# Optimization experiments

Measured on AMD Instinct MI355X. Metric: run time of the kernel, lower is better.

Reference implementation:

```python
import jax, jax.numpy as jnp
import numpy as np


def _register_translation(target_images, src_images, upsample_factor):
    # squeeze channel dim -> (B, H, W), promote to complex for FFT
    tgt = target_images[..., 0].astype(jnp.complex64)
    src = src_images[..., 0].astype(jnp.complex64)
    B, H, W = tgt.shape

    target_freq = jnp.fft.fft2(tgt)
    src_freq = jnp.fft.fft2(src)
    # cross-power spectrum (skimage register_translation convention)
    image_product = src_freq * jnp.conj(target_freq)
    cross_corr = jnp.fft.ifft2(image_product)

    # coarse (integer-pixel) peak
    abs_cc = jnp.abs(cross_corr).reshape(B, -1)
    idx = jnp.argmax(abs_cc, axis=1)
    maxima = jnp.stack([idx // W, idx % W], axis=1).astype(jnp.float32)  # (B,2)
    shape_f = jnp.array([H, W], jnp.float32)
    midpoints = jnp.array([H // 2, W // 2], jnp.float32)  # fix(axis_size/2)
    shifts = jnp.where(maxima > midpoints, maxima - shape_f, maxima)

    if upsample_factor > 1:
        uf = float(upsample_factor)
        shifts = jnp.round(shifts * uf) / uf
        region = int(np.ceil(upsample_factor * 1.5))  # upsampled region size
        dftshift = float(np.fix(region / 2.0))
        offsets = dftshift - shifts * uf  # (B,2) sample region offsets

        r_idx = jnp.arange(region, dtype=jnp.float32)
        freq_r = (jnp.fft.fftfreq(H) * H).astype(jnp.float32)  # ifftshift(arange(H)-H//2)
        freq_c = (jnp.fft.fftfreq(W) * W).astype(jnp.float32)
        two_pi = 2.0 * np.pi

        # per-batch small DFT kernels: row (B, region, H), col (B, W, region)
        row_ang = (two_pi / (H * uf)) * (r_idx[None, :, None] - offsets[:, 0][:, None, None]) * freq_r[None, None, :]
        col_ang = (two_pi / (W * uf)) * freq_c[None, :, None] * (r_idx[None, None, :] - offsets[:, 1][:, None, None])
        row_k = jnp.exp(-1j * row_ang)
        col_k = jnp.exp(-1j * col_ang)

        # upsampled DFT of conj(image_product), then conjugate back
        cc_up = jnp.conj(jnp.einsum('brh,bhw,bwc->brc', row_k, jnp.conj(image_product), col_k))
        abs_up = jnp.abs(cc_up).reshape(B, -1)
        idx2 = jnp.argmax(abs_up, axis=1)
        max2 = jnp.stack([idx2 // region, idx2 % region], axis=1).astype(jnp.float32) - dftshift
        shifts = shifts + max2 / uf

    return shifts  # (B, 2) -- (row_shift, col_shift)


def setup_inputs() -> dict:
    key = jax.random.key(0)
    k1, k2 = jax.random.split(key)
    B, H, W = 32, 512, 512
    target_images = jax.random.normal(k1, (B, H, W, 1), dtype=jnp.float32)
    src_images = jax.random.normal(k2, (B, H, W, 1), dtype=jnp.float32)
    return {"target_images": target_images, "src_images": src_images, "upsample_factor": 20}


def reference(target_images, src_images, upsample_factor):
    return _register_translation(target_images, src_images, upsample_factor)
```

## Files before the change

kernel.cpp:

```cpp
#include <hip/hip_runtime.h>
#include <math.h>

#define BN 32
#define HN 512
#define WN 512
#define REGION 30
#define RPAD 32
#define UFV 20.0f
#define DFTSHIFT 15.0f
#define TWO_PI 6.2831853071795864769f
#define HS 8
#define HCH (HN / HS)
#define WS 8
#define WCH (WN / WS)

typedef float2 cplx;

__device__ __forceinline__ cplx cmul(cplx a, cplx b){
    return make_float2(a.x*b.x - a.y*b.y, a.x*b.y + a.y*b.x);
}
__device__ __forceinline__ cplx cadd(cplx a, cplx b){
    return make_float2(a.x + b.x, a.y + b.y);
}
__device__ __forceinline__ cplx csub(cplx a, cplx b){
    return make_float2(a.x - b.x, a.y - b.y);
}
__device__ __forceinline__ int brev9(int i){ return (int)(__brev((unsigned)i) >> 23); }
__device__ __forceinline__ int brev6(int i){ return (int)(__brev((unsigned)i) >> 26); }
__device__ __forceinline__ int csl(int h, int c){ return c * 546 + h + (h >> 4); }

#define BFLY(a,b,w){ cplx t_ = cmul(w,b); b = make_float2(a.x - t_.x, a.y - t_.y); a = cadd(a, t_); }
#define BFLY1(a,b){ cplx t_ = b; b = make_float2(a.x - t_.x, a.y - t_.y); a = cadd(a, t_); }

__device__ __forceinline__ void fft512_regs(cplx* v, const float2* tw, cplx* ds, int lane){
    const cplx wI  = *(const cplx*)&tw[128];
    const cplx w8a = *(const cplx*)&tw[64];
    const cplx w8b = *(const cplx*)&tw[192];
    BFLY1(v[0],v[1]); BFLY1(v[2],v[3]); BFLY1(v[4],v[5]); BFLY1(v[6],v[7]);
    BFLY1(v[0],v[2]); BFLY(v[1],v[3],wI); BFLY1(v[4],v[6]); BFLY(v[5],v[7],wI);
    BFLY1(v[0],v[4]); BFLY(v[1],v[5],w8a); BFLY(v[2],v[6],wI); BFLY(v[3],v[7],w8b);
    const int h = lane >> 3, lo = lane & 7;
    const int bw = 9 * lane;
    const int br = 72 * h + lo;
    #pragma unroll
    for (int j = 0; j < 8; ++j) ds[bw + j] = v[j];
    asm volatile("s_waitcnt lgkmcnt(0)" ::: "memory");
    #pragma unroll
    for (int j = 0; j < 8; ++j) v[j] = ds[br + 9*j];
    {
        cplx wA = *(const cplx*)&tw[lo<<5];
        BFLY(v[0],v[1],wA); BFLY(v[2],v[3],wA); BFLY(v[4],v[5],wA); BFLY(v[6],v[7],wA);
        cplx wB0 = *(const cplx*)&tw[lo<<4], wB1 = *(const cplx*)&tw[128+(lo<<4)];
        BFLY(v[0],v[2],wB0); BFLY(v[1],v[3],wB1); BFLY(v[4],v[6],wB0); BFLY(v[5],v[7],wB1);
        cplx wC0 = *(const cplx*)&tw[lo<<3], wC1 = *(const cplx*)&tw[64+(lo<<3)];
        cplx wC2 = *(const cplx*)&tw[128+(lo<<3)], wC3 = *(const cplx*)&tw[192+(lo<<3)];
        BFLY(v[0],v[4],wC0); BFLY(v[1],v[5],wC1); BFLY(v[2],v[6],wC2); BFLY(v[3],v[7],wC3);
    }
    #pragma unroll
    for (int j = 0; j < 8; ++j) ds[br + 9*j] = v[j];
    asm volatile("s_waitcnt lgkmcnt(0)" ::: "memory");
    const int br3 = lane + (lane >> 3);
    #pragma unroll
    for (int j = 0; j < 8; ++j) v[j] = ds[br3 + 72*j];
    {
        cplx wD = *(const cplx*)&tw[lane<<2];
        BFLY(v[0],v[1],wD); BFLY(v[2],v[3],wD); BFLY(v[4],v[5],wD); BFLY(v[6],v[7],wD);
        cplx wE0 = *(const cplx*)&tw[lane<<1], wE1 = *(const cplx*)&tw[128+(lane<<1)];
        BFLY(v[0],v[2],wE0); BFLY(v[1],v[3],wE1); BFLY(v[4],v[6],wE0); BFLY(v[5],v[7],wE1);
        cplx wF0 = *(const cplx*)&tw[lane], wF1 = *(const cplx*)&tw[64+lane];
        cplx wF2 = *(const cplx*)&tw[128+lane], wF3 = *(const cplx*)&tw[192+lane];
        BFLY(v[0],v[4],wF0); BFLY(v[1],v[5],wF1); BFLY(v[2],v[6],wF2); BFLY(v[3],v[7],wF3);
    }
}

__global__ void __launch_bounds__(256) row_fft_pack(const float* __restrict__ tgt,
                                                    const float* __restrict__ src,
                                                    cplx* __restrict__ Fz){
    __shared__ float2 tw[256];
    __shared__ cplx ds[4 * 576];
    const int tid = threadIdx.x;
    { float sv, cv; sincosf(-TWO_PI * (float)tid * (1.0f/512.0f), &sv, &cv);
      tw[tid] = make_float2(cv, sv); }
    __syncthreads();
    const int wave = tid >> 6, lane = tid & 63;
    const int rid = blockIdx.x * 4 + wave;
    const float* tr = tgt + (size_t)rid * WN;
    const float* sr = src + (size_t)rid * WN;
    const int rb6 = brev6(lane);
    const int B3[8] = {0,256,128,384,64,320,192,448};
    cplx v[8];
    #pragma unroll
    for (int j = 0; j < 8; ++j){ int o = B3[j] + rb6; v[j] = make_float2(tr[o], sr[o]); }
    fft512_regs(v, (const float2*)tw, ds + wave * 576, lane);
    cplx* orow = Fz + (size_t)rid * WN;
    #pragma unroll
    for (int j = 0; j < 8; ++j) orow[64*j + lane] = v[j];
}

__device__ __forceinline__ void col_fft8(cplx* sm, const float2* tw, int tid){
    const cplx wI  = tw[128];
    const cplx w8a = tw[64];
    const cplx w8b = tw[192];
    const int c  = tid & 7;
    const int k0 = tid >> 3, k1 = k0 + 32;
    const int B3[8] = {0,256,128,384,64,320,192,448};
    cplx ya[8], yb[8];
    {
        const int r0 = brev6(k0), r1 = brev6(k1);
        #pragma unroll
        for (int m = 0; m < 8; ++m){
            ya[m] = sm[csl(B3[m] + r0, c)];
            yb[m] = sm[csl(B3[m] + r1, c)];
        }
    }
    __syncthreads();
    #define P0(x) \
        BFLY1(x[0],x[1]); BFLY1(x[2],x[3]); BFLY1(x[4],x[5]); BFLY1(x[6],x[7]); \
        BFLY1(x[0],x[2]); BFLY(x[1],x[3],wI); BFLY1(x[4],x[6]); BFLY(x[5],x[7],wI); \
        BFLY1(x[0],x[4]); BFLY(x[1],x[5],w8a); BFLY(x[2],x[6],wI); BFLY(x[3],x[7],w8b);
    P0(ya); P0(yb);
    #undef P0
    #pragma unroll
    for (int m = 0; m < 8; ++m){
        sm[csl(8*k0 + m, c)] = ya[m];
        sm[csl(8*k1 + m, c)] = yb[m];
    }
    __syncthreads();
    #pragma unroll
    for (int pass = 1; pass < 3; ++pass){
        const int st = 3*pass + 1;
        const int h1 = 1 << (st - 1);
        #pragma unroll
        for (int gi = 0; gi < 2; ++gi){
            const int k = (tid >> 3) + 32*gi;
            const int q = k & (h1 - 1);
            const int i0 = ((k >> (st - 1)) << (st + 2)) + q;
            cplx x[8];
            #pragma unroll
            for (int m = 0; m < 8; ++m) x[m] = sm[csl(i0 + m*h1, c)];
            cplx w1 = tw[q << (9 - st)];
            BFLY(x[0],x[1],w1); BFLY(x[2],x[3],w1); BFLY(x[4],x[5],w1); BFLY(x[6],x[7],w1);
            cplx w2a = tw[q << (8 - st)];
            cplx w2b = tw[(q << (8 - st)) + 128];
            BFLY(x[0],x[2],w2a); BFLY(x[1],x[3],w2b); BFLY(x[4],x[6],w2a); BFLY(x[5],x[7],w2b);
            cplx w30 = tw[q << (7 - st)];
            cplx w31 = tw[(q << (7 - st)) + 64];
            cplx w32 = tw[(q << (7 - st)) + 128];
            cplx w33 = tw[(q << (7 - st)) + 192];
            BFLY(x[0],x[4],w30); BFLY(x[1],x[5],w31); BFLY(x[2],x[6],w32); BFLY(x[3],x[7],w33);
            #pragma unroll
            for (int m = 0; m < 8; ++m) sm[csl(i0 + m*h1, c)] = x[m];
        }
        __syncthreads();
    }
}

__global__ void col_fft_fwd(cplx* __restrict__ buf){
    const int b  = blockIdx.y;
    const int w0 = blockIdx.x * 8;
    const int tid = threadIdx.x;
    __shared__ cplx sm[4368];
    __shared__ float2 tw[256];
    { float sv, cv; sincosf(-TWO_PI * (float)tid * (1.0f/512.0f), &sv, &cv);
      tw[tid] = make_float2(cv, sv); }
    cplx* base = buf + (size_t)b * HN * WN + w0;
    for (int idx = tid; idx < HN * 4; idx += 256){
        int h = idx >> 2, c2 = (idx & 3) << 1;
        float4 v = *(const float4*)(base + (size_t)h * WN + c2);
        sm[csl(h, c2)]     = make_float2(v.x, v.y);
        sm[csl(h, c2 + 1)] = make_float2(v.z, v.w);
    }
    __syncthreads();
    col_fft8(sm, (const float2*)tw, tid);
    for (int idx = tid; idx < HN * 4; idx += 256){
        int h = idx >> 2, c2 = (idx & 3) << 1;
        cplx a = sm[csl(h, c2)], d = sm[csl(h, c2 + 1)];
        *(float4*)(base + (size_t)h * WN + c2) = make_float4(a.x, a.y, d.x, d.y);
    }
}

__global__ void __launch_bounds__(256) cross_rowinv(cplx* __restrict__ Fz, cplx* __restrict__ cc){
    __shared__ float2 tw[256];
    __shared__ cplx ds[4 * 1184];
    const int tid = threadIdx.x;
    { float sv, cv; sincosf(TWO_PI * (float)tid * (1.0f/512.0f), &sv, &cv);
      tw[tid] = make_float2(cv, sv); }
    __syncthreads();
    const int wave = tid >> 6, lane = tid & 63;
    const int p = blockIdx.x * 4 + wave;
    if (p > 256) return;
    const int b = blockIdx.y;
    const int h1 = p, h2 = (HN - p) & (HN - 1);
    cplx* r1 = Fz + ((size_t)b * HN + h1) * WN;
    cplx* r2 = Fz + ((size_t)b * HN + h2) * WN;
    cplx* A = ds + wave * 1184;
    cplx* B = A + 592;
    #pragma unroll
    for (int u = 0; u < 8; ++u){
        A[lane + 64*u] = r1[lane + 64*u];
        B[lane + 64*u] = r2[lane + 64*u];
    }
    asm volatile("s_waitcnt lgkmcnt(0)" ::: "memory");
    const int rb6 = brev6(lane);
    const int B3[8] = {0,256,128,384,64,320,192,448};
    cplx v1[8], v2[8];
    #pragma unroll
    for (int j = 0; j < 8; ++j){
        int w  = B3[j] + rb6;
        int wm = (WN - w) & (WN - 1);
        cplx Aw = A[w], Bw = B[w], Am = A[wm], Bm = B[wm];
        { cplx Bc = make_float2(Bm.x, -Bm.y);
          cplx s = cadd(Aw, Bc);
          cplx d = make_float2(Aw.x - Bc.x, Aw.y - Bc.y);
          cplx D = make_float2(d.x*s.x + d.y*s.y, d.y*s.x - d.x*s.y);
          v1[j] = make_float2(0.25f * D.y, -0.25f * D.x); }
        { cplx Ac = make_float2(Am.x, -Am.y);
          cplx s = cadd(Bw, Ac);
          cplx d = make_float2(Bw.x - Ac.x, Bw.y - Ac.y);
          cplx D = make_float2(d.x*s.x + d.y*s.y, d.y*s.x - d.x*s.y);
          v2[j] = make_float2(0.25f * D.y, -0.25f * D.x); }
        r1[w] = v1[j];
        r2[w] = v2[j];
    }
    fft512_regs(v1, (const float2*)tw, A, lane);
    fft512_regs(v2, (const float2*)tw, B, lane);
    cplx* c1 = cc + ((size_t)b * HN + h1) * WN;
    cplx* c2 = cc + ((size_t)b * HN + h2) * WN;
    #pragma unroll
    for (int j = 0; j < 8; ++j){ c1[64*j + lane] = v1[j]; c2[64*j + lane] = v2[j]; }
}

__global__ void colinv_argmax(const cplx* __restrict__ buf, float2* __restrict__ cand){
    const int b  = blockIdx.y;
    const int w0 = blockIdx.x * 8;
    const int tid = threadIdx.x;
    __shared__ cplx sm[4368];
    __shared__ float2 tw[256];
    { float sv, cv; sincosf(TWO_PI * (float)tid * (1.0f/512.0f), &sv, &cv);
      tw[tid] = make_float2(cv, sv); }
    const cplx* base = buf + (size_t)b * HN * WN + w0;
    for (int idx = tid; idx < HN * 4; idx += 256){
        int h = idx >> 2, c2 = (idx & 3) << 1;
        float4 v = *(const float4*)(base + (size_t)h * WN + c2);
        sm[csl(h, c2)]     = make_float2(v.x, v.y);
        sm[csl(h, c2 + 1)] = make_float2(v.z, v.w);
    }
    __syncthreads();
    col_fft8(sm, (const float2*)tw, tid);
    float best = -1.0f; int bidx = 0x7fffffff;
    for (int idx = tid; idx < HN * 8; idx += 256){
        int h = idx >> 3, c = idx & 7;
        cplx v = sm[csl(h, c)];
        float mm = v.x * v.x + v.y * v.y;
        if (mm > best){ best = mm; bidx = h * WN + w0 + c; }
    }
    __shared__ float vals[256];
    __shared__ int   idxs[256];
    vals[tid] = best; idxs[tid] = bidx;
    __syncthreads();
    for (int s = 128; s > 0; s >>= 1){
        if (tid < s){
            if (vals[tid + s] > vals[tid] ||
                (vals[tid + s] == vals[tid] && idxs[tid + s] < idxs[tid])){
                vals[tid] = vals[tid + s]; idxs[tid] = idxs[tid + s];
            }
        }
        __syncthreads();
    }
    if (tid == 0) cand[b * 64 + blockIdx.x] = make_float2(vals[0], __int_as_float(idxs[0]));
}

__global__ void coarse_reduce(const float2* __restrict__ cand, float* __restrict__ small){
    const int b = blockIdx.x, t = threadIdx.x;
    float2 c = cand[b * 64 + t];
    float v = c.x; int ix = __float_as_int(c.y);
    for (int off = 32; off > 0; off >>= 1){
        float v2 = __shfl_down(v, off);
        int   i2 = __shfl_down(ix, off);
        if (v2 > v || (v2 == v && i2 < ix)){ v = v2; ix = i2; }
    }
    if (t == 0){
        int row = ix / WN, col = ix % WN;
        float sr = (row > HN / 2) ? (float)(row - HN) : (float)row;
        float sc = (col > WN / 2) ? (float)(col - WN) : (float)col;
        small[b * 4 + 0] = sr;
        small[b * 4 + 1] = sc;
        small[b * 4 + 2] = DFTSHIFT - sr * UFV;
        small[b * 4 + 3] = DFTSHIFT - sc * UFV;
    }
}

__global__ void __launch_bounds__(256, 3) upsample_T(const cplx* __restrict__ P,
                                                     const float* __restrict__ small,
                                                     cplx* __restrict__ Tpart){
    const int b = blockIdx.y, hs = blockIdx.z;
    const int tid = threadIdx.x;
    const int wp = tid & 31;
    const int rbase = tid >> 5;
    const int w = blockIdx.x * 64 + wp * 2;
    const int h0 = hs * HCH;
    const float off0 = small[b * 4 + 2];
    const float CC = TWO_PI / (HN * UFV);
    __shared__ float2 rk[RPAD][HCH];
    for (int idx = tid; idx < RPAD * HCH; idx += 256){
        int r = idx >> 6, hh = idx & (HCH - 1);
        int h = h0 + hh;
        float fr = (h < HN / 2) ? (float)h : (float)(h - HN);
        float sv, cv; sincosf(-CC * ((float)r - off0) * fr, &sv, &cv);
        rk[r][hh] = make_float2(cv, sv);
    }
    __syncthreads();
    cplx a0[4], a1[4];
    #pragma unroll
    for (int u = 0; u < 4; ++u){ a0[u] = make_float2(0.f,0.f); a1[u] = make_float2(0.f,0.f); }
    const cplx* pc = P + ((size_t)b * HN + h0) * WN + w;

    float4 pvA[4], pvB[4];
    #pragma unroll
    for (int k = 0; k < 4; ++k) pvA[k] = *(const float4*)(pc + (size_t)k * WN);

    #pragma unroll 1
    for (int hh = 0; hh < HCH; hh += 8){
        #pragma unroll
        for (int k = 0; k < 4; ++k)
            pvB[k] = *(const float4*)(pc + (size_t)(hh + 4 + k) * WN);
        #pragma unroll
        for (int k = 0; k < 4; ++k){
            #pragma unroll
            for (int u = 0; u < 4; ++u){
                cplx wv = rk[rbase * 4 + u][hh + k];
                a0[u].x += wv.x * pvA[k].x + wv.y * pvA[k].y;
                a0[u].y += wv.y * pvA[k].x - wv.x * pvA[k].y;
                a1[u].x += wv.x * pvA[k].z + wv.y * pvA[k].w;
                a1[u].y += wv.y * pvA[k].z - wv.x * pvA[k].w;
            }
        }
        if (hh + 8 < HCH){
            #pragma unroll
            for (int k = 0; k < 4; ++k)
                pvA[k] = *(const float4*)(pc + (size_t)(hh + 8 + k) * WN);
        }
        #pragma unroll
        for (int k = 0; k < 4; ++k){
            #pragma unroll
            for (int u = 0; u < 4; ++u){
                cplx wv = rk[rbase * 4 + u][hh + 4 + k];
                a0[u].x += wv.x * pvB[k].x + wv.y * pvB[k].y;
                a0[u].y += wv.y * pvB[k].x - wv.x * pvB[k].y;
                a1[u].x += wv.x * pvB[k].z + wv.y * pvB[k].w;
                a1[u].y += wv.y * pvB[k].z - wv.x * pvB[k].w;
            }
        }
    }

    #pragma unroll
    for (int u = 0; u < 4; ++u){
        int r = rbase * 4 + u;
        if (r < REGION){
            float4* dst = (float4*)(Tpart + (((size_t)hs * BN + b) * REGION + r) * WN + w);
            *dst = make_float4(a0[u].x, a0[u].y, a1[u].x, a1[u].y);
        }
    }
}

__global__ void upsample_U_part(const cplx* __restrict__ Tpart, const float* __restrict__ small,
                                cplx* __restrict__ Upart){
    const int ws = blockIdx.x, b = blockIdx.y;
    const int tid = threadIdx.x;
    const int w0 = ws * WCH;
    const float off1 = small[b * 4 + 3];
    const float CC = TWO_PI / (WN * UFV);
    __shared__ float2 Ts[REGION][WCH];
    __shared__ float2 ck[WCH][REGION];
    const size_t TS = (size_t)BN * REGION * WN;
    for (int idx = tid; idx < REGION * WCH; idx += 256){
        int r = idx >> 6, ww = idx & (WCH - 1);
        cplx s = make_float2(0.f, 0.f);
        #pragma unroll
        for (int hs = 0; hs < HS; ++hs)
            s = cadd(s, Tpart[(size_t)hs * TS + ((size_t)b * REGION + r) * WN + w0 + ww]);
        Ts[r][ww] = s;
    }
    for (int idx = tid; idx < WCH * REGION; idx += 256){
        int ww = idx / REGION, c = idx - ww * REGION;
        int w = w0 + ww;
        float fw = (w < WN / 2) ? (float)w : (float)(w - WN);
        float sv, cv; sincosf(-CC * fw * ((float)c - off1), &sv, &cv);
        ck[ww][c] = make_float2(cv, sv);
    }
    __syncthreads();
    #pragma unroll
    for (int q = 0; q < 4; ++q){
        int o = tid + 256 * q;
        if (o < REGION * REGION){
            int r = o / REGION, c = o - r * REGION;
            cplx acc = make_float2(0.f, 0.f);
            #pragma unroll
            for (int ww = 0; ww < WCH; ++ww)
                acc = cadd(acc, cmul(Ts[r][ww], ck[ww][c]));
            Upart[((size_t)ws * BN + b) * (REGION * REGION) + o] = acc;
        }
    }
}

__global__ void upsample_argmax(const cplx* __restrict__ Upart, const float* __restrict__ small,
                                float* __restrict__ out){
    const int b = blockIdx.x;
    const int tid = threadIdx.x;
    float best = -1.0f; int bidx = 0x7fffffff;
    #pragma unroll
    for (int q = 0; q < 4; ++q){
        int o = tid + 256 * q;
        if (o < REGION * REGION){
            cplx u = make_float2(0.f, 0.f);
            #pragma unroll
            for (int ws = 0; ws < WS; ++ws)
                u = cadd(u, Upart[((size_t)ws * BN + b) * (REGION * REGION) + o]);
            float m = u.x * u.x + u.y * u.y;
            if (m > best){ best = m; bidx = o; }
        }
    }
    __shared__ float vals[256];
    __shared__ int   idxs[256];
    vals[tid] = best; idxs[tid] = bidx;
    __syncthreads();
    for (int s = 128; s > 0; s >>= 1){
        if (tid < s){
            if (vals[tid + s] > vals[tid] ||
                (vals[tid + s] == vals[tid] && idxs[tid + s] < idxs[tid])){
                vals[tid] = vals[tid + s]; idxs[tid] = idxs[tid + s];
            }
        }
        __syncthreads();
    }
    if (tid == 0){
        int o = idxs[0];
        float r = (float)(o / REGION) - DFTSHIFT;
        float c = (float)(o % REGION) - DFTSHIFT;
        out[b * 2 + 0] = small[b * 4 + 0] + r / UFV;
        out[b * 2 + 1] = small[b * 4 + 1] + c / UFV;
    }
}

extern "C" void kernel_launch(void* const* d_in, const int* in_sizes, int n_in,
                              void* d_out, int out_size, void* d_ws, size_t ws_size,
                              hipStream_t stream){
    const float* tgt = (const float*)d_in[0];
    const float* src = (const float*)d_in[1];
    float* out = (float*)d_out;

    const size_t BIG = (size_t)BN * HN * WN;
    cplx* buf1 = (cplx*)d_ws;
    cplx* buf2 = buf1 + BIG;
    float* small = (float*)(buf2 + BIG);
    float2* cand = (float2*)(small + 128);

    const size_t TSTRIDE = (size_t)BN * REGION * WN;
    cplx* Tpart = buf2;
    cplx* Upart = buf2 + HS * TSTRIDE;

    dim3 blk(256);
    row_fft_pack<<<dim3(BN * HN / 4), blk, 0, stream>>>(tgt, src, buf1);
    col_fft_fwd<<<dim3(WN / 8, BN), blk, 0, stream>>>(buf1);
    cross_rowinv<<<dim3((257 + 3) / 4, BN), blk, 0, stream>>>(buf1, buf2);
    colinv_argmax<<<dim3(WN / 8, BN), blk, 0, stream>>>(buf2, cand);
    coarse_reduce<<<dim3(BN), dim3(64), 0, stream>>>(cand, small);
    upsample_T<<<dim3(WN / 64, BN, HS), blk, 0, stream>>>(buf1, small, Tpart);
    upsample_U_part<<<dim3(WS, BN), blk, 0, stream>>>(Tpart, small, Upart);
    upsample_argmax<<<dim3(BN), blk, 0, stream>>>(Upart, small, out);
}
```

Before: 202.5 us.

## Exploit Hermitian symmetry to halve row inverse FFT and upsample DFT work

The product spectrum of two real images is Hermitian, so the inverse row FFT for row h2 is taken as the conjugate of row h1's result instead of being computed separately, which halves that kernel's FFT work. The upsampled DFT likewise uses conjugate symmetry: only the first half of the columns (plus the Nyquist column and row) is processed, and the other half is folded in through real-part doubling and a correction term. This cuts the grid of upsample_T and upsample_U_part roughly in half. The cost is more intricate index and edge handling, and correctness now depends on the real-input assumption.

```diff
diff --git a/kernel.cpp b/kernel.cpp
--- a/kernel.cpp
+++ b/kernel.cpp
@@ -11,8 +11,7 @@
 #define TWO_PI 6.2831853071795864769f
 #define HS 8
 #define HCH (HN / HS)
-#define WS 8
-#define WCH (WN / WS)
+#define WS 4
 
 typedef float2 cplx;
 
@@ -203,7 +202,7 @@
     asm volatile("s_waitcnt lgkmcnt(0)" ::: "memory");
     const int rb6 = brev6(lane);
     const int B3[8] = {0,256,128,384,64,320,192,448};
-    cplx v1[8], v2[8];
+    cplx v1[8];
     #pragma unroll
     for (int j = 0; j < 8; ++j){
         int w  = B3[j] + rb6;
@@ -218,16 +217,18 @@
           cplx s = cadd(Bw, Ac);
           cplx d = make_float2(Bw.x - Ac.x, Bw.y - Ac.y);
           cplx D = make_float2(d.x*s.x + d.y*s.y, d.y*s.x - d.x*s.y);
-          v2[j] = make_float2(0.25f * D.y, -0.25f * D.x); }
+          r2[w] = make_float2(0.25f * D.y, -0.25f * D.x); }
         r1[w] = v1[j];
-        r2[w] = v2[j];
     }
     fft512_regs(v1, (const float2*)tw, A, lane);
-    fft512_regs(v2, (const float2*)tw, B, lane);
     cplx* c1 = cc + ((size_t)b * HN + h1) * WN;
-    cplx* c2 = cc + ((size_t)b * HN + h2) * WN;
-    #pragma unroll
-    for (int j = 0; j < 8; ++j){ c1[64*j + lane] = v1[j]; c2[64*j + lane] = v2[j]; }
+    #pragma unroll
+    for (int j = 0; j < 8; ++j) c1[64*j + lane] = v1[j];
+    if (h2 != h1){
+        cplx* c2 = cc + ((size_t)b * HN + h2) * WN;
+        #pragma unroll
+        for (int j = 0; j < 8; ++j) c2[64*j + lane] = make_float2(v1[j].x, -v1[j].y);
+    }
 }
 
 __global__ void colinv_argmax(const cplx* __restrict__ buf, float2* __restrict__ cand){
@@ -363,42 +364,69 @@
     }
 }
 
-__global__ void upsample_U_part(const cplx* __restrict__ Tpart, const float* __restrict__ small,
-                                cplx* __restrict__ Upart){
+__global__ void upsample_U_part(const cplx* __restrict__ Tpart, const cplx* __restrict__ P,
+                                const float* __restrict__ small, cplx* __restrict__ Upart){
     const int ws = blockIdx.x, b = blockIdx.y;
     const int tid = threadIdx.x;
-    const int w0 = ws * WCH;
+    const int w0 = ws * 64;
+    const float off0 = small[b * 4 + 2];
     const float off1 = small[b * 4 + 3];
-    const float CC = TWO_PI / (WN * UFV);
-    __shared__ float2 Ts[REGION][WCH];
-    __shared__ float2 ck[WCH][REGION];
+    const float CW = TWO_PI / (WN * UFV);
+    const float CH = TWO_PI / (HN * UFV);
+    __shared__ float2 Ts[REGION][64];
+    __shared__ float2 ck[64][REGION];
+    __shared__ float2 p256[64];
+    __shared__ float2 T256s[REGION];
     const size_t TS = (size_t)BN * REGION * WN;
-    for (int idx = tid; idx < REGION * WCH; idx += 256){
-        int r = idx >> 6, ww = idx & (WCH - 1);
+    for (int idx = tid; idx < REGION * 64; idx += 256){
+        int r = idx >> 6, ww = idx & 63;
         cplx s = make_float2(0.f, 0.f);
         #pragma unroll
         for (int hs = 0; hs < HS; ++hs)
             s = cadd(s, Tpart[(size_t)hs * TS + ((size_t)b * REGION + r) * WN + w0 + ww]);
         Ts[r][ww] = s;
     }
-    for (int idx = tid; idx < WCH * REGION; idx += 256){
+    if (tid < 64) p256[tid] = P[((size_t)b * HN + 256) * WN + w0 + tid];
+    if (ws == 0 && tid >= 64 && tid < 64 + REGION){
+        int r = tid - 64;
+        cplx s = make_float2(0.f, 0.f);
+        #pragma unroll
+        for (int hs = 0; hs < HS; ++hs)
+            s = cadd(s, Tpart[(size_t)hs * TS + ((size_t)b * REGION + r) * WN + 256]);
+        T256s[r] = s;
+    }
+    for (int idx = tid; idx < 64 * REGION; idx += 256){
         int ww = idx / REGION, c = idx - ww * REGION;
         int w = w0 + ww;
-        float fw = (w < WN / 2) ? (float)w : (float)(w - WN);
-        float sv, cv; sincosf(-CC * fw * ((float)c - off1), &sv, &cv);
+        float sv, cv; sincosf(-CW * (float)w * ((float)c - off1), &sv, &cv);
         ck[ww][c] = make_float2(cv, sv);
     }
     __syncthreads();
+    const int start = (ws == 0) ? 1 : 0;
     #pragma unroll
     for (int q = 0; q < 4; ++q){
         int o = tid + 256 * q;
         if (o < REGION * REGION){
             int r = o / REGION, c = o - r * REGION;
-            cplx acc = make_float2(0.f, 0.f);
-            #pragma unroll
-            for (int ww = 0; ww < WCH; ++ww)
-                acc = cadd(acc, cmul(Ts[r][ww], ck[ww][c]));
-            Upart[((size_t)ws * BN + b) * (REGION * REGION) + o] = acc;
+            float racc = 0.f;
+            cplx s2 = make_float2(0.f, 0.f);
+            for (int ww = start; ww < 64; ++ww){
+                float2 T = Ts[r][ww], K = ck[ww][c];
+                racc += T.x * K.x - T.y * K.y;
+                float2 pv = p256[ww];
+                s2.x += pv.x * K.x + pv.y * K.y;
+                s2.y += pv.y * K.x - pv.x * K.y;
+            }
+            float th = CH * ((float)r - off0) * 256.0f;
+            float snt = sinf(th);
+            cplx contrib = make_float2(2.f * racc - 2.f * snt * s2.y,
+                                       2.f * snt * s2.x);
+            if (ws == 0){
+                contrib = cadd(contrib, Ts[r][0]);
+                float s256, c256; sincosf(CW * 256.0f * ((float)c - off1), &s256, &c256);
+                contrib = cadd(contrib, cmul(T256s[r], make_float2(c256, s256)));
+            }
+            Upart[((size_t)ws * BN + b) * (REGION * REGION) + o] = contrib;
         }
     }
 }
@@ -465,7 +493,7 @@
     cross_rowinv<<<dim3((257 + 3) / 4, BN), blk, 0, stream>>>(buf1, buf2);
     colinv_argmax<<<dim3(WN / 8, BN), blk, 0, stream>>>(buf2, cand);
     coarse_reduce<<<dim3(BN), dim3(64), 0, stream>>>(cand, small);
-    upsample_T<<<dim3(WN / 64, BN, HS), blk, 0, stream>>>(buf1, small, Tpart);
-    upsample_U_part<<<dim3(WS, BN), blk, 0, stream>>>(Tpart, small, Upart);
+    upsample_T<<<dim3(5, BN, HS), blk, 0, stream>>>(buf1, small, Tpart);
+    upsample_U_part<<<dim3(WS, BN), blk, 0, stream>>>(Tpart, buf1, small, Upart);
     upsample_argmax<<<dim3(BN), blk, 0, stream>>>(Upart, small, out);
 }
```

New measurement: 193.3 us. -4.5%, faster.
